# Kernel tuning notes

Hardware: AMD Instinct MI355X
Metric: run time of the kernel (lower is better)

Reference implementation:

```python
import jax, jax.numpy as jnp
import numpy as np

NUM_BLOCKS = 8
SPARSITY_THRESHOLD = 0.01
HARD_THRESHOLDING_FRACTION = 1.0
SCALE = 0.02


def setup_inputs() -> dict:
    key = jax.random.key(0)
    k_x, k_w1, k_b1, k_w2, k_b2 = jax.random.split(key, 5)
    B, C, H, W = 1, 768, 180, 360
    bs = C // NUM_BLOCKS  # block_size = 96
    x = jax.random.normal(k_x, (B, C, H, W), dtype=jnp.float32)
    w1 = SCALE * jax.random.normal(k_w1, (NUM_BLOCKS, bs, bs, 2), dtype=jnp.float32)
    b1 = SCALE * jax.random.normal(k_b1, (NUM_BLOCKS, bs, 1, 1, 2), dtype=jnp.float32)
    w2 = SCALE * jax.random.normal(k_w2, (NUM_BLOCKS, bs, bs, 2), dtype=jnp.float32)
    b2 = SCALE * jax.random.normal(k_b2, (NUM_BLOCKS, bs, 1, 1, 2), dtype=jnp.float32)
    return {"x": x, "w1": w1, "b1": b1, "w2": w2, "b2": b2}


def _compl_mul_add(a, b, c):
    # a: [B,k,i,X,Y,2(re/im)], b: [k,i,o,2], c: [k,o,1,1,2]
    tmp = jnp.einsum('bkixys,kiot->stbkoxy', a, b)
    re = tmp[0, 0] - tmp[1, 1]
    im = tmp[1, 0] + tmp[0, 1]
    return jnp.stack([re, im], axis=-1) + c


def _softshrink(v, lam):
    return jnp.sign(v) * jnp.maximum(jnp.abs(v) - lam, 0.0)


def reference(x, w1, b1, w2, b2):
    bias = x
    B, C, H, W = x.shape
    bs = C // NUM_BLOCKS
    total_modes = H // 2 + 1
    kept_modes = int(total_modes * HARD_THRESHOLDING_FRACTION)

    xf = jnp.fft.rfft2(x.astype(jnp.float32), s=(H, W), axes=(-2, -1), norm='ortho')
    xf = xf.reshape(B, NUM_BLOCKS, bs, H, W // 2 + 1)
    xr = jnp.stack([xf.real, xf.imag], axis=-1)  # [B,k,i,H,Wf,2]

    lo = total_modes - kept_modes
    hi = total_modes + kept_modes  # python slice clips at H, same as torch
    a = xr[:, :, :, lo:hi, :kept_modes, :]
    o1 = jax.nn.relu(_compl_mul_add(a, w1, b1))
    o2 = jnp.zeros_like(xr).at[:, :, :, lo:hi, :kept_modes, :].set(
        _compl_mul_add(o1, w2, b2))

    s = _softshrink(o2, SPARSITY_THRESHOLD)
    xc = (s[..., 0] + 1j * s[..., 1]).reshape(B, C, H, W // 2 + 1)
    out = jnp.fft.irfft2(xc, s=(H, W), axes=(-2, -1), norm='ortho').astype(bias.dtype)
    return out + bias
```

## Files before the change

### kernel.cpp

```cpp
#include <hip/hip_runtime.h>
#include <math.h>


#define R360f 0.05270462766947299f
#define R180f 0.07453559924999299f
#define LAM   0.01f

typedef short v8s __attribute__((ext_vector_type(8)));
typedef float v4f __attribute__((ext_vector_type(4)));

#define MFMA(a,b,c) __builtin_amdgcn_mfma_f32_16x16x32_bf16(a,b,c,0,0,0)

#define NBUF  26542080
#define OBA   (2*NBUF)
#define OBH   (OBA + 73728)
#define OBHI  (OBH + 147456)
#define OBW1  (OBHI + 147456)
#define OBW2  (OBW1 + 294912)
#define OBE   (OBW2 + 294912)
#define NBAKE 1032192

static __device__ __forceinline__ short f2bs(float f){
    unsigned u = __builtin_bit_cast(unsigned, f);
    u = (u + 0x7fffu + ((u >> 16) & 1u)) >> 16;
    return (short)u;
}
static __device__ __forceinline__ v8s ld8(const short* p){
    return __builtin_bit_cast(v8s, *(const uint4*)p);
}
union PK { short s[4]; uint2 u; };
static __device__ __forceinline__ uint2 pk4(v4f a){
    PK t; t.s[0]=f2bs(a[0]); t.s[1]=f2bs(a[1]); t.s[2]=f2bs(a[2]); t.s[3]=f2bs(a[3]);
    return t.u;
}
union S8 { uint4 u; short s[8]; v8s v; };
static __device__ __forceinline__ float sshrink(float v){
    return (v > LAM) ? (v - LAM) : ((v < -LAM) ? (v + LAM) : 0.f);
}

__global__ __launch_bounds__(256) void bake(const float* __restrict__ w1,
                                            const float* __restrict__ w2,
                                            short* __restrict__ bt){
    int idx = blockIdx.x*256 + threadIdx.x;
    if (idx >= NBAKE) return;
    float v = 0.f;
    if (idx < 73728){
        int n = idx/384, k = idx - n*384;
        int s = n >= 96, y = n - s*96;
        if (y < 91 && k < 360){
            float th = (float)((k*y) % 360) * 0.017453292519943295f;
            float sv, cv; sincosf(th, &sv, &cv);
            v = s ? -sv*R360f : cv*R360f;
        }
        bt[OBA + idx] = f2bs(v); return;
    }
    idx -= 73728;
    if (idx < 147456){
        int m = idx/384, k = idx - m*384;
        int s = m >= 192, hp = m - s*192;
        if (hp < 180 && k < 360){
            int si = k >= 180; int h = k - si*180;
            float th = (float)((h*hp) % 180) * 0.03490658503988659f;
            float sv, cv; sincosf(th, &sv, &cv);
            v = R180f * (s == 0 ? (si == 0 ? cv : sv) : (si == 0 ? -sv : cv));
        }
        bt[OBH + idx] = f2bs(v); return;
    }
    idx -= 147456;
    if (idx < 147456){
        int n = idx/384, k = idx - n*384;
        int s = n >= 192, h = n - s*192;
        if (h < 180 && k < 360){
            int sp = k >= 180; int hp = k - sp*180;
            float th = (float)((h*hp) % 180) * 0.03490658503988659f;
            float sv, cv; sincosf(th, &sv, &cv);
            v = R180f * (s == 0 ? (sp == 0 ? cv : -sv) : (sp == 0 ? sv : cv));
        }
        bt[OBHI + idx] = f2bs(v); return;
    }
    idx -= 147456;
    if (idx < 294912){
        int kb = idx / 36864; int r = idx - kb*36864;
        int n = r / 192, k = r - n*192;
        int o = n >> 1, sp = n & 1, i = k >> 1, si = k & 1;
        const float* wp = w1 + ((((kb*96 + i)*96) + o) << 1);
        v = sp == 0 ? (si == 0 ? wp[0] : -wp[1]) : (si == 0 ? wp[1] : wp[0]);
        bt[OBW1 + idx] = f2bs(v); return;
    }
    idx -= 294912;
    if (idx < 294912){
        int kb = idx / 36864; int r = idx - kb*36864;
        int n = r / 192, k = r - n*192;
        int o = n >> 1, sp = n & 1, i = k >> 1, si = k & 1;
        const float* wp = w2 + ((((kb*96 + i)*96) + o) << 1);
        v = sp == 0 ? (si == 0 ? wp[0] : -wp[1]) : (si == 0 ? wp[1] : wp[0]);
        bt[OBW2 + idx] = f2bs(v); return;
    }
    idx -= 294912;
    {
        int w = idx / 192, k = idx - w*192;
        int s = k >= 96, y = k - s*96;
        if (w < 360 && y < 91){
            float th = (float)((y*w) % 360) * 0.017453292519943295f;
            float sv, cv; sincosf(th, &sv, &cv);
            v = (s == 0) ? (y == 0 ? 1.f : 2.f) * cv * R360f
                         : (y == 0 ? 0.f : -2.f*sv*R360f);
        }
        bt[OBE + idx] = f2bs(v);
    }
}

__global__ __launch_bounds__(256) void gA(const float* __restrict__ x,
                                          short* __restrict__ G1,
                                          const short* __restrict__ BA){
    const int b = blockIdx.x, c = b >> 1, hh = (b & 1)*96;
    const int tid = threadIdx.x, wid = tid >> 6, lane = tid & 63;
    const int l15 = lane & 15, q8 = (lane >> 4) << 3, q4 = q8 >> 1;
    const int nt0 = wid*3;
    const v4f vz = {0.f,0.f,0.f,0.f};
    v4f acc[6][3];
    #pragma unroll
    for (int i=0;i<6;++i){ acc[i][0]=vz; acc[i][1]=vz; acc[i][2]=vz; }
    for (int ks=0; ks<12; ++ks){
        const int k0 = ks*32;
        int kk = k0 + q8; if (kk >= 360) kk = 0;
        v8s af[6];
        #pragma unroll
        for (int mt=0; mt<6; ++mt){
            int h = hh + mt*16 + l15; if (h > 179) h = 179;
            const float* xp = x + (c*180 + h)*360 + kk;
            float4 f0 = *(const float4*)xp;
            float4 f1 = *(const float4*)(xp + 4);
            S8 tt;
            tt.s[0]=f2bs(f0.x); tt.s[1]=f2bs(f0.y); tt.s[2]=f2bs(f0.z); tt.s[3]=f2bs(f0.w);
            tt.s[4]=f2bs(f1.x); tt.s[5]=f2bs(f1.y); tt.s[6]=f2bs(f1.z); tt.s[7]=f2bs(f1.w);
            af[mt] = tt.v;
        }
        v8s bf[3];
        #pragma unroll
        for (int j=0;j<3;++j)
            bf[j] = ld8(BA + ((nt0+j)*16 + l15)*384 + k0 + q8);
        #pragma unroll
        for (int mt=0; mt<6; ++mt)
            #pragma unroll
            for (int j=0;j<3;++j)
                acc[mt][j] = MFMA(af[mt], bf[j], acc[mt][j]);
    }
    #pragma unroll
    for (int mt=0; mt<6; ++mt){
        int hg = hh + mt*16 + q4;
        if (hg >= 180) continue;
        #pragma unroll
        for (int j=0;j<3;++j){
            int n = (nt0+j)*16 + l15;
            int s = n >= 96, y = n - s*96;
            *(uint2*)(G1 + (c*96 + y)*360 + s*180 + hg) = pk4(acc[mt][j]);
        }
    }
}

__global__ __launch_bounds__(512) void gHf(const short* __restrict__ G1,
                                           short* __restrict__ F2,
                                           const short* __restrict__ BH){
    const int c = blockIdx.x;
    const int tid = threadIdx.x, wid = tid >> 6, lane = tid & 63;
    const int l15 = lane & 15, q8 = (lane >> 4) << 3, q4 = q8 >> 1;
    const int mt0 = wid*3;
    const v4f vz = {0.f,0.f,0.f,0.f};
    v4f acc[3][6];
    #pragma unroll
    for (int i=0;i<3;++i)
        #pragma unroll
        for (int j=0;j<6;++j) acc[i][j]=vz;
    for (int ks=0; ks<12; ++ks){
        const int k0 = ks*32;
        int kk = k0 + q8; if (kk >= 360) kk = 0;
        v8s af[3];
        #pragma unroll
        for (int i=0;i<3;++i)
            af[i] = ld8(BH + ((mt0+i)*16 + l15)*384 + k0 + q8);
        v8s bf[6];
        #pragma unroll
        for (int j=0;j<6;++j)
            bf[j] = ld8(G1 + (c*96 + j*16 + l15)*360 + kk);
        #pragma unroll
        for (int i=0;i<3;++i)
            #pragma unroll
            for (int j=0;j<6;++j)
                acc[i][j] = MFMA(af[i], bf[j], acc[i][j]);
    }
    #pragma unroll
    for (int i=0;i<3;++i){
        int m = (mt0+i)*16 + q4;
        int s = m >= 192, hp = m - s*192;
        if (hp >= 180) continue;
        const int rb = (2*c + s)*17280 + hp;
        #pragma unroll
        for (int j=0;j<6;++j){
            int y = j*16 + l15;
            *(uint2*)(F2 + rb + y*180) = pk4(acc[i][j]);
        }
    }
}

__global__ __launch_bounds__(256) void gC(const short* __restrict__ F2,
                                          short* __restrict__ F3,
                                          const short* __restrict__ BW1,
                                          const short* __restrict__ BW2,
                                          const float* __restrict__ b1,
                                          const float* __restrict__ b2){
    __shared__ short Act[64*200];
    __shared__ short O1[64*200];
    const int mt = blockIdx.x, kb = blockIdx.y, m0 = mt*64;
    const int tid = threadIdx.x;
    #pragma unroll
    for (int i=0;i<6;++i){
        int ch = tid + 256*i;
        int qq = ch / 192, rr = ch - qq*192;
        S8 tt; tt.u = *(const uint4*)(F2 + (kb*192 + rr)*17280 + m0 + qq*8);
        #pragma unroll
        for (int j=0;j<8;++j) Act[(qq*8+j)*200 + rr] = tt.s[j];
    }
    __syncthreads();
    const int wid = tid >> 6, lane = tid & 63, l15 = lane & 15;
    const int q8 = (lane >> 4) << 3, q4 = q8 >> 1;
    const int nt0 = wid*3;
    const short* bw1 = BW1 + kb*36864;
    const short* bw2 = BW2 + kb*36864;
    const v4f vz = {0.f,0.f,0.f,0.f};
    v4f a1[4][3];
    #pragma unroll
    for (int mr=0;mr<4;++mr){ a1[mr][0]=vz; a1[mr][1]=vz; a1[mr][2]=vz; }
    for (int ks=0; ks<6; ++ks){
        const int k0 = ks*32 + q8;
        v8s af[4];
        #pragma unroll
        for (int mr=0;mr<4;++mr)
            af[mr] = __builtin_bit_cast(v8s, *(const uint4*)(Act + (mr*16 + l15)*200 + k0));
        v8s bf[3];
        #pragma unroll
        for (int j=0;j<3;++j)
            bf[j] = ld8(bw1 + ((nt0+j)*16 + l15)*192 + k0);
        #pragma unroll
        for (int mr=0;mr<4;++mr)
            #pragma unroll
            for (int j=0;j<3;++j)
                a1[mr][j] = MFMA(af[mr], bf[j], a1[mr][j]);
    }
    #pragma unroll
    for (int j=0;j<3;++j){
        int n = (nt0+j)*16 + l15;
        float bv = b1[(kb*96 + (n>>1))*2 + (n&1)];
        #pragma unroll
        for (int mr=0;mr<4;++mr)
            #pragma unroll
            for (int r=0;r<4;++r)
                O1[(mr*16 + q4 + r)*200 + n] = f2bs(fmaxf(a1[mr][j][r] + bv, 0.f));
    }
    __syncthreads();
    v4f a2[4][3];
    #pragma unroll
    for (int mr=0;mr<4;++mr){ a2[mr][0]=vz; a2[mr][1]=vz; a2[mr][2]=vz; }
    for (int ks=0; ks<6; ++ks){
        const int k0 = ks*32 + q8;
        v8s af[4];
        #pragma unroll
        for (int mr=0;mr<4;++mr)
            af[mr] = __builtin_bit_cast(v8s, *(const uint4*)(O1 + (mr*16 + l15)*200 + k0));
        v8s bf[3];
        #pragma unroll
        for (int j=0;j<3;++j)
            bf[j] = ld8(bw2 + ((nt0+j)*16 + l15)*192 + k0);
        #pragma unroll
        for (int mr=0;mr<4;++mr)
            #pragma unroll
            for (int j=0;j<3;++j)
                a2[mr][j] = MFMA(af[mr], bf[j], a2[mr][j]);
    }
    #pragma unroll
    for (int mr=0;mr<4;++mr){
        const int mb = m0 + mr*16 + q4;
        const int y = mb / 180, hp = mb - y*180;
        #pragma unroll
        for (int j=0;j<3;++j){
            int n = (nt0+j)*16 + l15;
            int o = n >> 1, sp = n & 1;
            float bv = b2[(kb*96 + o)*2 + sp];
            v4f vv;
            #pragma unroll
            for (int r=0;r<4;++r) vv[r] = sshrink(a2[mr][j][r] + bv);
            *(uint2*)(F3 + ((kb*96 + o)*96 + y)*360 + sp*180 + hp) = pk4(vv);
        }
    }
}

__global__ __launch_bounds__(512) void gHi(const short* __restrict__ F3,
                                           short* __restrict__ Sp,
                                           const short* __restrict__ BHI){
    const int c = blockIdx.x;
    const int tid = threadIdx.x, wid = tid >> 6, lane = tid & 63;
    const int l15 = lane & 15, q8 = (lane >> 4) << 3, q4 = q8 >> 1;
    const int nt0 = wid*3;
    const v4f vz = {0.f,0.f,0.f,0.f};
    v4f acc[6][3];
    #pragma unroll
    for (int i=0;i<6;++i){ acc[i][0]=vz; acc[i][1]=vz; acc[i][2]=vz; }
    for (int ks=0; ks<12; ++ks){
        const int k0 = ks*32;
        int kk = k0 + q8; if (kk >= 360) kk = 0;
        v8s af[6];
        #pragma unroll
        for (int i=0;i<6;++i)
            af[i] = ld8(F3 + (c*96 + i*16 + l15)*360 + kk);
        v8s bf[3];
        #pragma unroll
        for (int j=0;j<3;++j)
            bf[j] = ld8(BHI + ((nt0+j)*16 + l15)*384 + k0 + q8);
        #pragma unroll
        for (int i=0;i<6;++i)
            #pragma unroll
            for (int j=0;j<3;++j)
                acc[i][j] = MFMA(af[i], bf[j], acc[i][j]);
    }
    #pragma unroll
    for (int j=0;j<3;++j){
        int n = (nt0+j)*16 + l15;
        int s = n >= 192, h = n - s*192;
        if (h >= 180) continue;
        const int rb = (c*180 + h)*192 + s*96;
        #pragma unroll
        for (int i=0;i<6;++i)
            *(uint2*)(Sp + rb + i*16 + q4) = pk4(acc[i][j]);
    }
}

__global__ __launch_bounds__(512, 2) void gE(const float* __restrict__ x,
                                             const short* __restrict__ Sp,
                                             const short* __restrict__ BE,
                                             float* __restrict__ out){
    const int b = blockIdx.x;
    const int tid = threadIdx.x, wid = tid >> 6, lane = tid & 63;
    const int l15 = lane & 15, q8 = (lane >> 4) << 3, q4 = q8 >> 1;
    const int R0 = b*128 + (wid >> 2)*64;
    const int qt = wid & 3;
    v4f acc[4][6];
    #pragma unroll
    for (int r=0;r<4;++r){
        const int rbase = (R0 + r*16 + l15)*360;
        #pragma unroll
        for (int j=0;j<6;++j){
            const int w0 = (qt*6 + j)*16 + q4;
            if (w0 < 360){
                float4 xv = *(const float4*)(x + rbase + w0);
                acc[r][j][0]=xv.x; acc[r][j][1]=xv.y; acc[r][j][2]=xv.z; acc[r][j][3]=xv.w;
            } else {
                acc[r][j] = (v4f){0.f,0.f,0.f,0.f};
            }
        }
    }
    const short* Sr = Sp + (R0 + l15)*192;
    const short* Bq = BE + (qt*96 + l15)*192;
    #pragma unroll
    for (int ks=0; ks<6; ++ks){
        const int k0 = ks*32 + q8;
        v8s af[6];
        #pragma unroll
        for (int j=0;j<6;++j) af[j] = ld8(Bq + j*3072 + k0);
        v8s bf[4];
        #pragma unroll
        for (int r=0;r<4;++r) bf[r] = ld8(Sr + r*3072 + k0);
        #pragma unroll
        for (int r=0;r<4;++r)
            #pragma unroll
            for (int j=0;j<6;++j)
                acc[r][j] = MFMA(af[j], bf[r], acc[r][j]);
    }
    #pragma unroll
    for (int r=0;r<4;++r){
        const int rbase = (R0 + r*16 + l15)*360;
        #pragma unroll
        for (int j=0;j<6;++j){
            const int w0 = (qt*6 + j)*16 + q4;
            if (w0 < 360)
                *(float4*)(out + rbase + w0) =
                    make_float4(acc[r][j][0], acc[r][j][1], acc[r][j][2], acc[r][j][3]);
        }
    }
}

extern "C" void kernel_launch(void* const* d_in, const int* in_sizes, int n_in,
                              void* d_out, int out_size, void* d_ws, size_t ws_size,
                              hipStream_t stream){
    const float* x  = (const float*)d_in[0];
    const float* w1 = (const float*)d_in[1];
    const float* b1 = (const float*)d_in[2];
    const float* w2 = (const float*)d_in[3];
    const float* b2 = (const float*)d_in[4];
    float* out = (float*)d_out;
    short* ws = (short*)d_ws;
    short* B1 = ws;
    short* B2 = ws + NBUF;

    hipLaunchKernelGGL(bake, dim3((NBAKE+255)/256), dim3(256), 0, stream, w1, w2, ws);
    hipLaunchKernelGGL(gA,  dim3(1536),    dim3(256), 0, stream, x, B1, ws + OBA);
    hipLaunchKernelGGL(gHf, dim3(768),     dim3(512), 0, stream, B1, B2, ws + OBH);
    hipLaunchKernelGGL(gC,  dim3(270, 8),  dim3(256), 0, stream, B2, B1,
                       ws + OBW1, ws + OBW2, b1, b2);
    hipLaunchKernelGGL(gHi, dim3(768),     dim3(512), 0, stream, B1, B2, ws + OBHI);
    hipLaunchKernelGGL(gE,  dim3(1080),    dim3(512), 0, stream, x, B2, ws + OBE, out);
}
```

Measured before the change: 733.7 us.

## Stage per-block input tiles in LDS for the three DFT GEMM kernels

In gA, gHf and gHi the whole 96-row input tile is now loaded once into shared memory (padded row stride 392, wrapped columns beyond 360) and the MFMA A/B fragments are read from LDS instead of repeated strided global loads. In gA this also converts x to bf16 once during staging rather than once per k-step per wave. The aim is to cut redundant global and L2 traffic across the waves of a block. The cost is about 75 KB of LDS per block, which lowers occupancy, plus a barrier before compute.

```diff
diff --git a/kernel.cpp b/kernel.cpp
--- a/kernel.cpp
+++ b/kernel.cpp
@@ -26,6 +26,9 @@
     return (short)u;
 }
 static __device__ __forceinline__ v8s ld8(const short* p){
+    return __builtin_bit_cast(v8s, *(const uint4*)p);
+}
+static __device__ __forceinline__ v8s ld8s(const short* p){
     return __builtin_bit_cast(v8s, *(const uint4*)p);
 }
 union PK { short s[4]; uint2 u; };
@@ -113,33 +116,37 @@
 __global__ __launch_bounds__(256) void gA(const float* __restrict__ x,
                                           short* __restrict__ G1,
                                           const short* __restrict__ BA){
+    __shared__ short X[96*392];
     const int b = blockIdx.x, c = b >> 1, hh = (b & 1)*96;
     const int tid = threadIdx.x, wid = tid >> 6, lane = tid & 63;
     const int l15 = lane & 15, q8 = (lane >> 4) << 3, q4 = q8 >> 1;
     const int nt0 = wid*3;
+    #pragma unroll
+    for (int i=0;i<36;++i){
+        int idx = tid + 256*i;
+        int row = idx / 96, ch = idx - row*96;
+        int col = ch*4;
+        int cc = col < 360 ? col : col - 360;
+        int h = hh + row; if (h > 179) h = 179;
+        float4 f = *(const float4*)(x + (c*180 + h)*360 + cc);
+        PK t; t.s[0]=f2bs(f.x); t.s[1]=f2bs(f.y); t.s[2]=f2bs(f.z); t.s[3]=f2bs(f.w);
+        *(uint2*)(X + row*392 + col) = t.u;
+    }
+    __syncthreads();
     const v4f vz = {0.f,0.f,0.f,0.f};
     v4f acc[6][3];
     #pragma unroll
     for (int i=0;i<6;++i){ acc[i][0]=vz; acc[i][1]=vz; acc[i][2]=vz; }
     for (int ks=0; ks<12; ++ks){
-        const int k0 = ks*32;
-        int kk = k0 + q8; if (kk >= 360) kk = 0;
+        const int k0 = ks*32 + q8;
         v8s af[6];
         #pragma unroll
-        for (int mt=0; mt<6; ++mt){
-            int h = hh + mt*16 + l15; if (h > 179) h = 179;
-            const float* xp = x + (c*180 + h)*360 + kk;
-            float4 f0 = *(const float4*)xp;
-            float4 f1 = *(const float4*)(xp + 4);
-            S8 tt;
-            tt.s[0]=f2bs(f0.x); tt.s[1]=f2bs(f0.y); tt.s[2]=f2bs(f0.z); tt.s[3]=f2bs(f0.w);
-            tt.s[4]=f2bs(f1.x); tt.s[5]=f2bs(f1.y); tt.s[6]=f2bs(f1.z); tt.s[7]=f2bs(f1.w);
-            af[mt] = tt.v;
-        }
+        for (int mt=0; mt<6; ++mt)
+            af[mt] = ld8s(X + (mt*16 + l15)*392 + k0);
         v8s bf[3];
         #pragma unroll
         for (int j=0;j<3;++j)
-            bf[j] = ld8(BA + ((nt0+j)*16 + l15)*384 + k0 + q8);
+            bf[j] = ld8(BA + ((nt0+j)*16 + l15)*384 + k0);
         #pragma unroll
         for (int mt=0; mt<6; ++mt)
             #pragma unroll
@@ -162,10 +169,20 @@
 __global__ __launch_bounds__(512) void gHf(const short* __restrict__ G1,
                                            short* __restrict__ F2,
                                            const short* __restrict__ BH){
+    __shared__ short G[96*392];
     const int c = blockIdx.x;
     const int tid = threadIdx.x, wid = tid >> 6, lane = tid & 63;
     const int l15 = lane & 15, q8 = (lane >> 4) << 3, q4 = q8 >> 1;
     const int mt0 = wid*3;
+    #pragma unroll
+    for (int i=0;i<9;++i){
+        int idx = tid + 512*i;
+        int row = idx / 48, ch = idx - row*48;
+        int col = ch*8;
+        int cc = col < 360 ? col : col - 360;
+        *(uint4*)(G + row*392 + col) = *(const uint4*)(G1 + (c*96 + row)*360 + cc);
+    }
+    __syncthreads();
     const v4f vz = {0.f,0.f,0.f,0.f};
     v4f acc[3][6];
     #pragma unroll
@@ -173,16 +190,15 @@
         #pragma unroll
         for (int j=0;j<6;++j) acc[i][j]=vz;
     for (int ks=0; ks<12; ++ks){
-        const int k0 = ks*32;
-        int kk = k0 + q8; if (kk >= 360) kk = 0;
+        const int k0 = ks*32 + q8;
         v8s af[3];
         #pragma unroll
         for (int i=0;i<3;++i)
-            af[i] = ld8(BH + ((mt0+i)*16 + l15)*384 + k0 + q8);
+            af[i] = ld8(BH + ((mt0+i)*16 + l15)*384 + k0);
         v8s bf[6];
         #pragma unroll
         for (int j=0;j<6;++j)
-            bf[j] = ld8(G1 + (c*96 + j*16 + l15)*360 + kk);
+            bf[j] = ld8s(G + (j*16 + l15)*392 + k0);
         #pragma unroll
         for (int i=0;i<3;++i)
             #pragma unroll
@@ -297,25 +313,34 @@
 __global__ __launch_bounds__(512) void gHi(const short* __restrict__ F3,
                                            short* __restrict__ Sp,
                                            const short* __restrict__ BHI){
+    __shared__ short F[96*392];
     const int c = blockIdx.x;
     const int tid = threadIdx.x, wid = tid >> 6, lane = tid & 63;
     const int l15 = lane & 15, q8 = (lane >> 4) << 3, q4 = q8 >> 1;
     const int nt0 = wid*3;
+    #pragma unroll
+    for (int i=0;i<9;++i){
+        int idx = tid + 512*i;
+        int row = idx / 48, ch = idx - row*48;
+        int col = ch*8;
+        int cc = col < 360 ? col : col - 360;
+        *(uint4*)(F + row*392 + col) = *(const uint4*)(F3 + (c*96 + row)*360 + cc);
+    }
+    __syncthreads();
     const v4f vz = {0.f,0.f,0.f,0.f};
     v4f acc[6][3];
     #pragma unroll
     for (int i=0;i<6;++i){ acc[i][0]=vz; acc[i][1]=vz; acc[i][2]=vz; }
     for (int ks=0; ks<12; ++ks){
-        const int k0 = ks*32;
-        int kk = k0 + q8; if (kk >= 360) kk = 0;
+        const int k0 = ks*32 + q8;
         v8s af[6];
         #pragma unroll
         for (int i=0;i<6;++i)
-            af[i] = ld8(F3 + (c*96 + i*16 + l15)*360 + kk);
+            af[i] = ld8s(F + (i*16 + l15)*392 + k0);
         v8s bf[3];
         #pragma unroll
         for (int j=0;j<3;++j)
-            bf[j] = ld8(BHI + ((nt0+j)*16 + l15)*384 + k0 + q8);
+            bf[j] = ld8(BHI + ((nt0+j)*16 + l15)*384 + k0);
         #pragma unroll
         for (int i=0;i<6;++i)
             #pragma unroll
```

Result: faster. 662.6 us (-9.7%).
